# Performance work log

Hardware: AMD Instinct MI355X
Metric: run time of the kernel (lower is better)

## Reference

```python
import jax, jax.numpy as jnp
import numpy as np

HIDDEN = 2048
NUM_HEADS = 32
NUM_GROUPS = 8
HEAD_DIM = HIDDEN // NUM_HEADS          # 64
GROUP_DIM = HEAD_DIM * NUM_GROUPS       # 512
HPG = NUM_HEADS // NUM_GROUPS           # heads per group = 4
B, S = 2, 2048


def setup_inputs() -> dict:
    key = jax.random.key(0)
    ks = jax.random.split(key, 6)
    sd = 1.0 / np.sqrt(HIDDEN)
    return {
        "x": jax.random.normal(ks[0], (B, S, HIDDEN), jnp.float32),
        "mask": jnp.ones((1, 1, S, S), jnp.int32),
        "Wq": jax.random.normal(ks[1], (HIDDEN, HIDDEN), jnp.float32) * sd,
        "bq": jnp.zeros((HIDDEN,), jnp.float32),
        "Wk": jax.random.normal(ks[2], (HIDDEN, GROUP_DIM), jnp.float32) * sd,
        "bk": jnp.zeros((GROUP_DIM,), jnp.float32),
        "Wv": jax.random.normal(ks[3], (HIDDEN, GROUP_DIM), jnp.float32) * sd,
        "bv": jnp.zeros((GROUP_DIM,), jnp.float32),
        "Wo": jax.random.normal(ks[4], (HIDDEN, HIDDEN), jnp.float32) * sd,
        "bo": jnp.zeros((HIDDEN,), jnp.float32),
    }


def reference(x, mask, Wq, bq, Wk, bk, Wv, bv, Wo, bo):
    b, s, _ = x.shape
    # projections
    q = x @ Wq + bq                                        # [B,S,H*d]
    k = x @ Wk + bk                                        # [B,S,G*d]
    v = x @ Wv + bv
    # split heads: q heads are group-major (g, p) to match the torch view
    q = q.reshape(b, s, NUM_GROUPS, HPG, HEAD_DIM)         # [B,S,G,P,d]
    k = k.reshape(b, s, NUM_GROUPS, HEAD_DIM)              # [B,S,G,d]
    v = v.reshape(b, s, NUM_GROUPS, HEAD_DIM)
    scale = 1.0 / np.sqrt(HEAD_DIM).astype(np.float32)
    # grouped attention without materializing repeated K/V
    scores = jnp.einsum('bsgpd,btgd->bgpst', q, k) * scale  # [B,G,P,S,T]
    if mask is not None:
        m = mask[:, :, None]                                # [1,1,1,S,T]
        scores = jnp.where(m == 0, jnp.float32(-1e9), scores)
    weights = jax.nn.softmax(scores, axis=-1)
    out = jnp.einsum('bgpst,btgd->bsgpd', weights, v)       # [B,S,G,P,d]
    out = out.reshape(b, s, HIDDEN)
    return out @ Wo + bo
```

## Files before the change

kernel.cpp:

```cpp
#include <hip/hip_runtime.h>
#include <hip/hip_bf16.h>


#define DEVINL __device__ __forceinline__

typedef __attribute__((ext_vector_type(8))) short bf16x8;
typedef __attribute__((ext_vector_type(4))) float f32x4;

DEVINL unsigned short f2bf(float f) {
  unsigned u = __builtin_bit_cast(unsigned, f);
  u += 0x7fffu + ((u >> 16) & 1u);
  return (unsigned short)(u >> 16);
}

DEVINL unsigned pk2bf(float a, float b) {
  __hip_bfloat162 h = __float22bfloat162_rn(float2{a, b});
  unsigned r;
  __builtin_memcpy(&r, &h, 4);
  return r;
}

DEVINL void gl_lds16(const void* g, void* l) {
  __builtin_amdgcn_global_load_lds(
      (const __attribute__((address_space(1))) void*)g,
      (__attribute__((address_space(3))) void*)l, 16, 0, 0);
}

__global__ __launch_bounds__(256)
void prep_k(const float* __restrict__ x,
            const float* __restrict__ Wq, const float* __restrict__ Wk,
            const float* __restrict__ Wv, const float* __restrict__ Wo,
            const int* __restrict__ mask,
            unsigned short* __restrict__ xb,
            unsigned short* __restrict__ WqT, unsigned short* __restrict__ WkT,
            unsigned short* __restrict__ WvT, unsigned short* __restrict__ WoT,
            int* __restrict__ flags)
{
  __shared__ float tile[64][68];
  __shared__ int fl[4];
  int blk = blockIdx.x;
  const int tid = threadIdx.x;
  if (blk < 4096) {
    size_t base = (size_t)blk * 2048 + tid * 8;
    float4 f0 = *(const float4*)&x[base];
    float4 f1 = *(const float4*)&x[base + 4];
    uint4 o;
    o.x = pk2bf(f0.x, f0.y); o.y = pk2bf(f0.z, f0.w);
    o.z = pk2bf(f1.x, f1.y); o.w = pk2bf(f1.z, f1.w);
    *(uint4*)&xb[base] = o;
    return;
  }
  blk -= 4096;
  if (blk >= 2560) {
    int fb = blk - 2560;
    int qt = fb >> 5, tt = fb & 31;
    bool hz = false;
#pragma unroll
    for (int it = 0; it < 8; ++it) {
      int l = it * 1024 + tid * 4;
      int row = l >> 6, col = l & 63;
      int4 mv = *(const int4*)&mask[(size_t)(qt * 128 + row) * 2048 + tt * 64 + col];
      hz |= (mv.x == 0) | (mv.y == 0) | (mv.z == 0) | (mv.w == 0);
    }
    unsigned long long bal = __ballot(hz);
    if ((tid & 63) == 0) fl[tid >> 6] = (bal != 0ull) ? 1 : 0;
    __syncthreads();
    if (tid == 0) flags[fb] = fl[0] | fl[1] | fl[2] | fl[3];
    return;
  }
  const float* W; unsigned short* WT; int N;
  if (blk < 1024)      { W = Wq; WT = WqT; N = 2048; }
  else if (blk < 1280) { W = Wk; WT = WkT; N = 512;  blk -= 1024; }
  else if (blk < 1536) { W = Wv; WT = WvT; N = 512;  blk -= 1280; }
  else                 { W = Wo; WT = WoT; N = 2048; blk -= 1536; }
  const int kt = blk & 31, nt = blk >> 5;
  const int k0 = kt * 64, n0 = nt * 64;
  const int tr = tid >> 4, tc4 = (tid & 15) * 4;
#pragma unroll
  for (int it = 0; it < 4; ++it) {
    int k = it * 16 + tr;
    float4 v = *(const float4*)&W[(size_t)(k0 + k) * N + n0 + tc4];
    tile[tc4 + 0][k] = v.x; tile[tc4 + 1][k] = v.y;
    tile[tc4 + 2][k] = v.z; tile[tc4 + 3][k] = v.w;
  }
  __syncthreads();
#pragma unroll
  for (int it = 0; it < 4; ++it) {
    int n = it * 16 + tr;
    uint2 o;
    o.x = pk2bf(tile[n][tc4 + 0], tile[n][tc4 + 1]);
    o.y = pk2bf(tile[n][tc4 + 2], tile[n][tc4 + 3]);
    *(uint2*)&WT[(size_t)(n0 + n) * 2048 + k0 + tc4] = o;
  }
}

template<int MODE>
__global__ __launch_bounds__(256)
void mm_k(const unsigned short* __restrict__ A,
          const unsigned short* __restrict__ B1,
          const unsigned short* __restrict__ B2,
          const float* __restrict__ bias1, const float* __restrict__ bias2,
          unsigned short* __restrict__ Ob, unsigned short* __restrict__ Ob2,
          float* __restrict__ Of)
{
  __shared__ __align__(16) unsigned short As[128 * 32];
  __shared__ __align__(16) unsigned short Bs[128 * 32];
  const int tid = threadIdx.x;
  const int lane = tid & 63, w = tid >> 6;
  const int l15 = lane & 15, quad = lane >> 4;
  const int wm = w & 1, wn = w >> 1;
  const int row0 = blockIdx.y * 128;
  const int col0 = blockIdx.x * 128;

  const bool second = (MODE == 1) && (col0 >= 512);
  const unsigned short* Bsrc = second ? B2 : B1;
  const float* bias = second ? bias2 : bias1;
  const int colB = second ? col0 - 512 : col0;

  f32x4 acc[4][4];
#pragma unroll
  for (int mt = 0; mt < 4; ++mt)
#pragma unroll
    for (int nt = 0; nt < 4; ++nt) acc[mt][nt] = (f32x4){0.f, 0.f, 0.f, 0.f};

  const int c0 = tid, c1 = 256 + tid;
  const size_t aoff0 = (size_t)(row0 + (c0 >> 2)) * 2048 + (c0 & 3) * 8;
  const size_t aoff1 = (size_t)(row0 + (c1 >> 2)) * 2048 + (c1 & 3) * 8;
  const size_t boff0 = (size_t)(colB + (c0 >> 2)) * 2048 + (c0 & 3) * 8;
  const size_t boff1 = (size_t)(colB + (c1 >> 2)) * 2048 + (c1 & 3) * 8;

  for (int k0 = 0; k0 < 2048; k0 += 32) {
    gl_lds16(A + aoff0 + k0, As + (size_t)c0 * 8);
    gl_lds16(A + aoff1 + k0, As + (size_t)c1 * 8);
    gl_lds16(Bsrc + boff0 + k0, Bs + (size_t)c0 * 8);
    gl_lds16(Bsrc + boff1 + k0, Bs + (size_t)c1 * 8);
    __syncthreads();
    bf16x8 af[4], bfr[4];
#pragma unroll
    for (int mt = 0; mt < 4; ++mt)
      af[mt] = *(const bf16x8*)&As[(wm * 64 + mt * 16 + l15) * 32 + quad * 8];
#pragma unroll
    for (int nt = 0; nt < 4; ++nt)
      bfr[nt] = *(const bf16x8*)&Bs[(wn * 64 + nt * 16 + l15) * 32 + quad * 8];
#pragma unroll
    for (int mt = 0; mt < 4; ++mt)
#pragma unroll
      for (int nt = 0; nt < 4; ++nt)
        acc[mt][nt] = __builtin_amdgcn_mfma_f32_16x16x32_bf16(
            af[mt], bfr[nt], acc[mt][nt], 0, 0, 0);
    __syncthreads();
  }

  const int rbase = row0 + wm * 64 + quad * 4;
#pragma unroll
  for (int nt = 0; nt < 4; ++nt) {
    const int cg = col0 + wn * 64 + nt * 16 + l15;
    const int cl = colB + wn * 64 + nt * 16 + l15;
    const float bv = bias[MODE == 1 ? cl : cg];
#pragma unroll
    for (int mt = 0; mt < 4; ++mt) {
#pragma unroll
      for (int reg = 0; reg < 4; ++reg) {
        const int r = rbase + mt * 16 + reg;
        const int bb = r >> 11, ss = r & 2047;
        float v = acc[mt][nt][reg] + bv;
        if constexpr (MODE == 0) {
          int g = cg >> 8, p = (cg >> 6) & 3, d = cg & 63;
          Ob[(((size_t)((bb * 8 + g) * 4 + p)) * 2048 + ss) * 64 + d] =
              f2bf(v * 0.1803368801111244f);
        } else if constexpr (MODE == 1) {
          int g = cl >> 6, d = cl & 63;
          if (!second)
            Ob[((size_t)(bb * 8 + g) * 2048 + ss) * 64 + d] = f2bf(v);
          else
            Ob2[((size_t)(bb * 8 + g) * 64 + d) * 2048 + ss] = f2bf(v);
        } else {
          Of[(size_t)r * 2048 + cg] = v;
        }
      }
    }
  }
}

__global__ __launch_bounds__(256)
void attn_k(const unsigned short* __restrict__ qb,
            const unsigned short* __restrict__ kb,
            const unsigned short* __restrict__ vb,
            const int* __restrict__ mask, const int* __restrict__ flags,
            unsigned short* __restrict__ attnb)
{
  __shared__ __align__(16) unsigned short Ks[64 * 64];
  __shared__ __align__(16) unsigned short Vs[64 * 64];
  __shared__ __align__(16) unsigned short Ps[128 * 72];
  const int tid = threadIdx.x;
  const int lane = tid & 63, w = tid >> 6;
  const int l15 = lane & 15, quad = lane >> 4;
  const int q0 = blockIdx.x * 128;
  const int bgp = blockIdx.y;
  const int b = bgp >> 5, bg = bgp >> 2, h = bgp & 31;

  const unsigned short* Qg = qb + (size_t)bgp * 2048 * 64;
  const unsigned short* Kg = kb + (size_t)bg * 2048 * 64;
  const unsigned short* Vg = vb + (size_t)bg * 64 * 2048;

  bf16x8 qf[2][2];
#pragma unroll
  for (int u = 0; u < 2; ++u) {
    const size_t qrow = (size_t)(q0 + w * 32 + u * 16 + l15) * 64;
    qf[u][0] = *(const bf16x8*)&Qg[qrow + quad * 8];
    qf[u][1] = *(const bf16x8*)&Qg[qrow + 32 + quad * 8];
  }

  float m_i[2] = {-3e38f, -3e38f}, l_p[2] = {0.f, 0.f};
  f32x4 acc_o[4][2];
#pragma unroll
  for (int dt = 0; dt < 4; ++dt)
#pragma unroll
    for (int u = 0; u < 2; ++u) acc_o[dt][u] = (f32x4){0.f, 0.f, 0.f, 0.f};

  const int c0 = tid, c1 = 256 + tid;
  const int kr0 = c0 >> 3, kx0 = ((c0 & 7) ^ (kr0 & 7)) * 8;
  const int kr1 = c1 >> 3, kx1 = ((c1 & 7) ^ (kr1 & 7)) * 8;

  for (int t0 = 0; t0 < 2048; t0 += 64) {
    __syncthreads();
    gl_lds16(Kg + (size_t)(t0 + kr0) * 64 + kx0, Ks + (size_t)c0 * 8);
    gl_lds16(Kg + (size_t)(t0 + kr1) * 64 + kx1, Ks + (size_t)c1 * 8);
    gl_lds16(Vg + (size_t)kr0 * 2048 + t0 + kx0, Vs + (size_t)c0 * 8);
    gl_lds16(Vg + (size_t)kr1 * 2048 + t0 + kx1, Vs + (size_t)c1 * 8);
    __syncthreads();

    f32x4 st[2][4];
#pragma unroll
    for (int nt = 0; nt < 4; ++nt) {
      const int trow = nt * 16 + l15, ks = trow & 7;
      bf16x8 k0f = *(const bf16x8*)&Ks[trow * 64 + ((quad ^ ks) * 8)];
      bf16x8 k1f = *(const bf16x8*)&Ks[trow * 64 + (((4 + quad) ^ ks) * 8)];
#pragma unroll
      for (int u = 0; u < 2; ++u) {
        f32x4 z = (f32x4){0.f, 0.f, 0.f, 0.f};
        z = __builtin_amdgcn_mfma_f32_16x16x32_bf16(k0f, qf[u][0], z, 0, 0, 0);
        st[u][nt] = __builtin_amdgcn_mfma_f32_16x16x32_bf16(k1f, qf[u][1], z, 0, 0, 0);
      }
    }

    if (flags[blockIdx.x * 32 + (t0 >> 6)]) {
#pragma unroll
      for (int u = 0; u < 2; ++u) {
        const size_t mrow = (size_t)(q0 + w * 32 + u * 16 + l15) * 2048;
#pragma unroll
        for (int nt = 0; nt < 4; ++nt) {
          int4 mv = *(const int4*)&mask[mrow + t0 + nt * 16 + quad * 4];
          if (mv.x == 0) st[u][nt][0] = -1e30f;
          if (mv.y == 0) st[u][nt][1] = -1e30f;
          if (mv.z == 0) st[u][nt][2] = -1e30f;
          if (mv.w == 0) st[u][nt][3] = -1e30f;
        }
      }
    }

#pragma unroll
    for (int u = 0; u < 2; ++u) {
      float bm = fmaxf(fmaxf(fmaxf(st[u][0][0], st[u][0][1]), fmaxf(st[u][0][2], st[u][0][3])),
                       fmaxf(fmaxf(st[u][1][0], st[u][1][1]), fmaxf(st[u][1][2], st[u][1][3])));
      float bm2 = fmaxf(fmaxf(fmaxf(st[u][2][0], st[u][2][1]), fmaxf(st[u][2][2], st[u][2][3])),
                        fmaxf(fmaxf(st[u][3][0], st[u][3][1]), fmaxf(st[u][3][2], st[u][3][3])));
      bm = fmaxf(bm, bm2);
      bm = fmaxf(bm, __shfl_xor(bm, 16, 64));
      bm = fmaxf(bm, __shfl_xor(bm, 32, 64));
      float mn = fmaxf(m_i[u], bm);
      float alpha = __builtin_amdgcn_exp2f(m_i[u] - mn);
      m_i[u] = mn;
      float sum = 0.f;
#pragma unroll
      for (int nt = 0; nt < 4; ++nt)
#pragma unroll
        for (int reg = 0; reg < 4; ++reg) {
          float p = __builtin_amdgcn_exp2f(st[u][nt][reg] - mn);
          st[u][nt][reg] = p;
          sum += p;
        }
      l_p[u] = l_p[u] * alpha + sum;
#pragma unroll
      for (int dt = 0; dt < 4; ++dt) {
        acc_o[dt][u][0] *= alpha; acc_o[dt][u][1] *= alpha;
        acc_o[dt][u][2] *= alpha; acc_o[dt][u][3] *= alpha;
      }
      const int srow = w * 32 + u * 16 + l15;
#pragma unroll
      for (int nt = 0; nt < 4; ++nt) {
        uint2 pkd;
        pkd.x = pk2bf(st[u][nt][0], st[u][nt][1]);
        pkd.y = pk2bf(st[u][nt][2], st[u][nt][3]);
        *(uint2*)&Ps[srow * 72 + nt * 16 + quad * 4] = pkd;
      }
    }
    asm volatile("s_waitcnt lgkmcnt(0)" ::: "memory");

    bf16x8 pf[2][2];
#pragma unroll
    for (int u = 0; u < 2; ++u) {
      const int srow = w * 32 + u * 16 + l15;
      pf[u][0] = *(const bf16x8*)&Ps[srow * 72 + quad * 8];
      pf[u][1] = *(const bf16x8*)&Ps[srow * 72 + 32 + quad * 8];
    }
#pragma unroll
    for (int dt = 0; dt < 4; ++dt) {
      const int drow = dt * 16 + l15, ks = drow & 7;
      bf16x8 v0 = *(const bf16x8*)&Vs[drow * 64 + ((quad ^ ks) * 8)];
      bf16x8 v1 = *(const bf16x8*)&Vs[drow * 64 + (((4 + quad) ^ ks) * 8)];
#pragma unroll
      for (int u = 0; u < 2; ++u) {
        acc_o[dt][u] = __builtin_amdgcn_mfma_f32_16x16x32_bf16(v0, pf[u][0], acc_o[dt][u], 0, 0, 0);
        acc_o[dt][u] = __builtin_amdgcn_mfma_f32_16x16x32_bf16(v1, pf[u][1], acc_o[dt][u], 0, 0, 0);
      }
    }
  }

#pragma unroll
  for (int u = 0; u < 2; ++u) {
    float l = l_p[u];
    l += __shfl_xor(l, 16, 64);
    l += __shfl_xor(l, 32, 64);
    const float inv = 1.0f / l;
    const int s = q0 + w * 32 + u * 16 + l15;
#pragma unroll
    for (int dt = 0; dt < 4; ++dt) {
      uint2 o;
      o.x = pk2bf(acc_o[dt][u][0] * inv, acc_o[dt][u][1] * inv);
      o.y = pk2bf(acc_o[dt][u][2] * inv, acc_o[dt][u][3] * inv);
      *(uint2*)&attnb[((size_t)(b * 2048 + s)) * 2048 + h * 64 + dt * 16 + quad * 4] = o;
    }
  }
}

extern "C" void kernel_launch(void* const* d_in, const int* in_sizes, int n_in,
                              void* d_out, int out_size, void* d_ws, size_t ws_size,
                              hipStream_t stream)
{
  (void)in_sizes; (void)n_in; (void)out_size; (void)ws_size;
  const float* x  = (const float*)d_in[0];
  const int* mask = (const int*)d_in[1];
  const float* Wq = (const float*)d_in[2];
  const float* bq = (const float*)d_in[3];
  const float* Wk = (const float*)d_in[4];
  const float* bk = (const float*)d_in[5];
  const float* Wv = (const float*)d_in[6];
  const float* bv = (const float*)d_in[7];
  const float* Wo = (const float*)d_in[8];
  const float* bo = (const float*)d_in[9];
  float* out = (float*)d_out;

  unsigned short* xb  = (unsigned short*)d_ws;
  unsigned short* WqT = xb  + 8388608;
  unsigned short* WkT = WqT + 4194304;
  unsigned short* WvT = WkT + 1048576;
  unsigned short* WoT = WvT + 1048576;
  unsigned short* qb  = WoT + 4194304;
  unsigned short* kb  = qb  + 8388608;
  unsigned short* vb  = kb  + 2097152;
  int* flags = (int*)(vb + 2097152);
  unsigned short* attnb = xb;

  dim3 blk(256);
  hipLaunchKernelGGL(prep_k, dim3(7168), blk, 0, stream,
                     x, Wq, Wk, Wv, Wo, mask, xb, WqT, WkT, WvT, WoT, flags);
  hipLaunchKernelGGL((mm_k<0>), dim3(16, 32), blk, 0, stream,
                     xb, WqT, (const unsigned short*)nullptr, bq, (const float*)nullptr,
                     qb, (unsigned short*)nullptr, (float*)nullptr);
  hipLaunchKernelGGL((mm_k<1>), dim3(8, 32), blk, 0, stream,
                     xb, WkT, WvT, bk, bv, kb, vb, (float*)nullptr);
  hipLaunchKernelGGL(attn_k, dim3(16, 64), blk, 0, stream,
                     qb, kb, vb, mask, flags, attnb);
  hipLaunchKernelGGL((mm_k<2>), dim3(16, 32), blk, 0, stream,
                     attnb, WoT, (const unsigned short*)nullptr, bo, (const float*)nullptr,
                     (unsigned short*)nullptr, (unsigned short*)nullptr, out);
}
```

Before: 411.6 us.

## Fuse QKV projection GEMMs, double-buffer attention K/V tiles, skip redundant softmax rescales

The separate Q and KV projection launches are merged into one 24x32-block GEMM over the contiguous WqT/WkT/WvT buffers. Each column block routes its bias and output layout by column range, which removes a launch and fills the GPU better. In attention, K/V tiles are double-buffered in LDS so the next tile's loads are issued while the current one is computed, at the cost of twice the LDS for K and V. The online-softmax rescale of the accumulator and running sum now runs only when some lane's running max increases, using a wave-uniform ballot.

```diff
diff --git a/kernel.cpp b/kernel.cpp
--- a/kernel.cpp
+++ b/kernel.cpp
@@ -94,14 +94,13 @@
   }
 }
 
-template<int MODE>
 __global__ __launch_bounds__(256)
-void mm_k(const unsigned short* __restrict__ A,
-          const unsigned short* __restrict__ B1,
-          const unsigned short* __restrict__ B2,
-          const float* __restrict__ bias1, const float* __restrict__ bias2,
-          unsigned short* __restrict__ Ob, unsigned short* __restrict__ Ob2,
-          float* __restrict__ Of)
+void mm_qkv(const unsigned short* __restrict__ A,
+            const unsigned short* __restrict__ Wt,
+            const float* __restrict__ bq, const float* __restrict__ bk,
+            const float* __restrict__ bv,
+            unsigned short* __restrict__ qb, unsigned short* __restrict__ kb,
+            unsigned short* __restrict__ vb)
 {
   __shared__ __align__(16) unsigned short As[128 * 32];
   __shared__ __align__(16) unsigned short Bs[128 * 32];
@@ -112,11 +111,6 @@
   const int row0 = blockIdx.y * 128;
   const int col0 = blockIdx.x * 128;
 
-  const bool second = (MODE == 1) && (col0 >= 512);
-  const unsigned short* Bsrc = second ? B2 : B1;
-  const float* bias = second ? bias2 : bias1;
-  const int colB = second ? col0 - 512 : col0;
-
   f32x4 acc[4][4];
 #pragma unroll
   for (int mt = 0; mt < 4; ++mt)
@@ -126,14 +120,14 @@
   const int c0 = tid, c1 = 256 + tid;
   const size_t aoff0 = (size_t)(row0 + (c0 >> 2)) * 2048 + (c0 & 3) * 8;
   const size_t aoff1 = (size_t)(row0 + (c1 >> 2)) * 2048 + (c1 & 3) * 8;
-  const size_t boff0 = (size_t)(colB + (c0 >> 2)) * 2048 + (c0 & 3) * 8;
-  const size_t boff1 = (size_t)(colB + (c1 >> 2)) * 2048 + (c1 & 3) * 8;
+  const size_t boff0 = (size_t)(col0 + (c0 >> 2)) * 2048 + (c0 & 3) * 8;
+  const size_t boff1 = (size_t)(col0 + (c1 >> 2)) * 2048 + (c1 & 3) * 8;
 
   for (int k0 = 0; k0 < 2048; k0 += 32) {
     gl_lds16(A + aoff0 + k0, As + (size_t)c0 * 8);
     gl_lds16(A + aoff1 + k0, As + (size_t)c1 * 8);
-    gl_lds16(Bsrc + boff0 + k0, Bs + (size_t)c0 * 8);
-    gl_lds16(Bsrc + boff1 + k0, Bs + (size_t)c1 * 8);
+    gl_lds16(Wt + boff0 + k0, Bs + (size_t)c0 * 8);
+    gl_lds16(Wt + boff1 + k0, Bs + (size_t)c1 * 8);
     __syncthreads();
     bf16x8 af[4], bfr[4];
 #pragma unroll
@@ -155,30 +149,94 @@
 #pragma unroll
   for (int nt = 0; nt < 4; ++nt) {
     const int cg = col0 + wn * 64 + nt * 16 + l15;
-    const int cl = colB + wn * 64 + nt * 16 + l15;
-    const float bv = bias[MODE == 1 ? cl : cg];
 #pragma unroll
     for (int mt = 0; mt < 4; ++mt) {
 #pragma unroll
       for (int reg = 0; reg < 4; ++reg) {
         const int r = rbase + mt * 16 + reg;
         const int bb = r >> 11, ss = r & 2047;
-        float v = acc[mt][nt][reg] + bv;
-        if constexpr (MODE == 0) {
+        float v = acc[mt][nt][reg];
+        if (col0 < 2048) {
+          v += bq[cg];
           int g = cg >> 8, p = (cg >> 6) & 3, d = cg & 63;
-          Ob[(((size_t)((bb * 8 + g) * 4 + p)) * 2048 + ss) * 64 + d] =
+          qb[(((size_t)((bb * 8 + g) * 4 + p)) * 2048 + ss) * 64 + d] =
               f2bf(v * 0.1803368801111244f);
-        } else if constexpr (MODE == 1) {
+        } else if (col0 < 2560) {
+          int cl = cg - 2048;
+          v += bk[cl];
           int g = cl >> 6, d = cl & 63;
-          if (!second)
-            Ob[((size_t)(bb * 8 + g) * 2048 + ss) * 64 + d] = f2bf(v);
-          else
-            Ob2[((size_t)(bb * 8 + g) * 64 + d) * 2048 + ss] = f2bf(v);
+          kb[((size_t)(bb * 8 + g) * 2048 + ss) * 64 + d] = f2bf(v);
         } else {
-          Of[(size_t)r * 2048 + cg] = v;
+          int cl = cg - 2560;
+          v += bv[cl];
+          int g = cl >> 6, d = cl & 63;
+          vb[((size_t)(bb * 8 + g) * 64 + d) * 2048 + ss] = f2bf(v);
         }
       }
     }
+  }
+}
+
+__global__ __launch_bounds__(256)
+void mm_out(const unsigned short* __restrict__ A,
+            const unsigned short* __restrict__ Bt,
+            const float* __restrict__ bias, float* __restrict__ Of)
+{
+  __shared__ __align__(16) unsigned short As[128 * 32];
+  __shared__ __align__(16) unsigned short Bs[128 * 32];
+  const int tid = threadIdx.x;
+  const int lane = tid & 63, w = tid >> 6;
+  const int l15 = lane & 15, quad = lane >> 4;
+  const int wm = w & 1, wn = w >> 1;
+  const int row0 = blockIdx.y * 128;
+  const int col0 = blockIdx.x * 128;
+
+  f32x4 acc[4][4];
+#pragma unroll
+  for (int mt = 0; mt < 4; ++mt)
+#pragma unroll
+    for (int nt = 0; nt < 4; ++nt) acc[mt][nt] = (f32x4){0.f, 0.f, 0.f, 0.f};
+
+  const int c0 = tid, c1 = 256 + tid;
+  const size_t aoff0 = (size_t)(row0 + (c0 >> 2)) * 2048 + (c0 & 3) * 8;
+  const size_t aoff1 = (size_t)(row0 + (c1 >> 2)) * 2048 + (c1 & 3) * 8;
+  const size_t boff0 = (size_t)(col0 + (c0 >> 2)) * 2048 + (c0 & 3) * 8;
+  const size_t boff1 = (size_t)(col0 + (c1 >> 2)) * 2048 + (c1 & 3) * 8;
+
+  for (int k0 = 0; k0 < 2048; k0 += 32) {
+    gl_lds16(A + aoff0 + k0, As + (size_t)c0 * 8);
+    gl_lds16(A + aoff1 + k0, As + (size_t)c1 * 8);
+    gl_lds16(Bt + boff0 + k0, Bs + (size_t)c0 * 8);
+    gl_lds16(Bt + boff1 + k0, Bs + (size_t)c1 * 8);
+    __syncthreads();
+    bf16x8 af[4], bfr[4];
+#pragma unroll
+    for (int mt = 0; mt < 4; ++mt)
+      af[mt] = *(const bf16x8*)&As[(wm * 64 + mt * 16 + l15) * 32 + quad * 8];
+#pragma unroll
+    for (int nt = 0; nt < 4; ++nt)
+      bfr[nt] = *(const bf16x8*)&Bs[(wn * 64 + nt * 16 + l15) * 32 + quad * 8];
+#pragma unroll
+    for (int mt = 0; mt < 4; ++mt)
+#pragma unroll
+      for (int nt = 0; nt < 4; ++nt)
+        acc[mt][nt] = __builtin_amdgcn_mfma_f32_16x16x32_bf16(
+            af[mt], bfr[nt], acc[mt][nt], 0, 0, 0);
+    __syncthreads();
+  }
+
+  const int rbase = row0 + wm * 64 + quad * 4;
+#pragma unroll
+  for (int nt = 0; nt < 4; ++nt) {
+    const int cg = col0 + wn * 64 + nt * 16 + l15;
+    const float bvv = bias[cg];
+#pragma unroll
+    for (int mt = 0; mt < 4; ++mt)
+#pragma unroll
+      for (int reg = 0; reg < 4; ++reg) {
+        const int r = rbase + mt * 16 + reg;
+        Of[(size_t)r * 2048 + cg] = acc[mt][nt][reg] + bvv;
+      }
   }
 }
 
@@ -189,8 +247,8 @@
             const int* __restrict__ mask, const int* __restrict__ flags,
             unsigned short* __restrict__ attnb)
 {
-  __shared__ __align__(16) unsigned short Ks[64 * 64];
-  __shared__ __align__(16) unsigned short Vs[64 * 64];
+  __shared__ __align__(16) unsigned short Ks[2 * 64 * 64];
+  __shared__ __align__(16) unsigned short Vs[2 * 64 * 64];
   __shared__ __align__(16) unsigned short Ps[128 * 72];
   const int tid = threadIdx.x;
   const int lane = tid & 63, w = tid >> 6;
@@ -222,20 +280,32 @@
   const int kr0 = c0 >> 3, kx0 = ((c0 & 7) ^ (kr0 & 7)) * 8;
   const int kr1 = c1 >> 3, kx1 = ((c1 & 7) ^ (kr1 & 7)) * 8;
 
+  gl_lds16(Kg + (size_t)kr0 * 64 + kx0, Ks + (size_t)c0 * 8);
+  gl_lds16(Kg + (size_t)kr1 * 64 + kx1, Ks + (size_t)c1 * 8);
+  gl_lds16(Vg + (size_t)kr0 * 2048 + kx0, Vs + (size_t)c0 * 8);
+  gl_lds16(Vg + (size_t)kr1 * 2048 + kx1, Vs + (size_t)c1 * 8);
+
   for (int t0 = 0; t0 < 2048; t0 += 64) {
-    __syncthreads();
-    gl_lds16(Kg + (size_t)(t0 + kr0) * 64 + kx0, Ks + (size_t)c0 * 8);
-    gl_lds16(Kg + (size_t)(t0 + kr1) * 64 + kx1, Ks + (size_t)c1 * 8);
-    gl_lds16(Vg + (size_t)kr0 * 2048 + t0 + kx0, Vs + (size_t)c0 * 8);
-    gl_lds16(Vg + (size_t)kr1 * 2048 + t0 + kx1, Vs + (size_t)c1 * 8);
-    __syncthreads();
+    const int cur = (t0 >> 6) & 1;
+    const unsigned short* Ksc = Ks + cur * 4096;
+    const unsigned short* Vsc = Vs + cur * 4096;
+    __syncthreads();
+    if (t0 + 64 < 2048) {
+      unsigned short* Ksn = Ks + (cur ^ 1) * 4096;
+      unsigned short* Vsn = Vs + (cur ^ 1) * 4096;
+      const int tn = t0 + 64;
+      gl_lds16(Kg + (size_t)(tn + kr0) * 64 + kx0, Ksn + (size_t)c0 * 8);
+      gl_lds16(Kg + (size_t)(tn + kr1) * 64 + kx1, Ksn + (size_t)c1 * 8);
+      gl_lds16(Vg + (size_t)kr0 * 2048 + tn + kx0, Vsn + (size_t)c0 * 8);
+      gl_lds16(Vg + (size_t)kr1 * 2048 + tn + kx1, Vsn + (size_t)c1 * 8);
+    }
 
     f32x4 st[2][4];
 #pragma unroll
     for (int nt = 0; nt < 4; ++nt) {
       const int trow = nt * 16 + l15, ks = trow & 7;
-      bf16x8 k0f = *(const bf16x8*)&Ks[trow * 64 + ((quad ^ ks) * 8)];
-      bf16x8 k1f = *(const bf16x8*)&Ks[trow * 64 + (((4 + quad) ^ ks) * 8)];
+      bf16x8 k0f = *(const bf16x8*)&Ksc[trow * 64 + ((quad ^ ks) * 8)];
+      bf16x8 k1f = *(const bf16x8*)&Ksc[trow * 64 + (((4 + quad) ^ ks) * 8)];
 #pragma unroll
       for (int u = 0; u < 2; ++u) {
         f32x4 z = (f32x4){0.f, 0.f, 0.f, 0.f};
@@ -268,24 +338,28 @@
       bm = fmaxf(bm, bm2);
       bm = fmaxf(bm, __shfl_xor(bm, 16, 64));
       bm = fmaxf(bm, __shfl_xor(bm, 32, 64));
-      float mn = fmaxf(m_i[u], bm);
-      float alpha = __builtin_amdgcn_exp2f(m_i[u] - mn);
-      m_i[u] = mn;
+      if (__ballot(bm > m_i[u])) {
+        float mn = fmaxf(m_i[u], bm);
+        float alpha = __builtin_amdgcn_exp2f(m_i[u] - mn);
+        m_i[u] = mn;
+        l_p[u] *= alpha;
+#pragma unroll
+        for (int dt = 0; dt < 4; ++dt) {
+          acc_o[dt][u][0] *= alpha; acc_o[dt][u][1] *= alpha;
+          acc_o[dt][u][2] *= alpha; acc_o[dt][u][3] *= alpha;
+        }
+      }
+      const float mm = m_i[u];
       float sum = 0.f;
 #pragma unroll
       for (int nt = 0; nt < 4; ++nt)
 #pragma unroll
         for (int reg = 0; reg < 4; ++reg) {
-          float p = __builtin_amdgcn_exp2f(st[u][nt][reg] - mn);
+          float p = __builtin_amdgcn_exp2f(st[u][nt][reg] - mm);
           st[u][nt][reg] = p;
           sum += p;
         }
-      l_p[u] = l_p[u] * alpha + sum;
-#pragma unroll
-      for (int dt = 0; dt < 4; ++dt) {
-        acc_o[dt][u][0] *= alpha; acc_o[dt][u][1] *= alpha;
-        acc_o[dt][u][2] *= alpha; acc_o[dt][u][3] *= alpha;
-      }
+      l_p[u] += sum;
       const int srow = w * 32 + u * 16 + l15;
 #pragma unroll
       for (int nt = 0; nt < 4; ++nt) {
@@ -307,8 +381,8 @@
 #pragma unroll
     for (int dt = 0; dt < 4; ++dt) {
       const int drow = dt * 16 + l15, ks = drow & 7;
-      bf16x8 v0 = *(const bf16x8*)&Vs[drow * 64 + ((quad ^ ks) * 8)];
-      bf16x8 v1 = *(const bf16x8*)&Vs[drow * 64 + (((4 + quad) ^ ks) * 8)];
+      bf16x8 v0 = *(const bf16x8*)&Vsc[drow * 64 + ((quad ^ ks) * 8)];
+      bf16x8 v1 = *(const bf16x8*)&Vsc[drow * 64 + (((4 + quad) ^ ks) * 8)];
 #pragma unroll
       for (int u = 0; u < 2; ++u) {
         acc_o[dt][u] = __builtin_amdgcn_mfma_f32_16x16x32_bf16(v0, pf[u][0], acc_o[dt][u], 0, 0, 0);
@@ -365,14 +439,10 @@
   dim3 blk(256);
   hipLaunchKernelGGL(prep_k, dim3(7168), blk, 0, stream,
                      x, Wq, Wk, Wv, Wo, mask, xb, WqT, WkT, WvT, WoT, flags);
-  hipLaunchKernelGGL((mm_k<0>), dim3(16, 32), blk, 0, stream,
-                     xb, WqT, (const unsigned short*)nullptr, bq, (const float*)nullptr,
-                     qb, (unsigned short*)nullptr, (float*)nullptr);
-  hipLaunchKernelGGL((mm_k<1>), dim3(8, 32), blk, 0, stream,
-                     xb, WkT, WvT, bk, bv, kb, vb, (float*)nullptr);
+  hipLaunchKernelGGL(mm_qkv, dim3(24, 32), blk, 0, stream,
+                     xb, WqT, bq, bk, bv, qb, kb, vb);
   hipLaunchKernelGGL(attn_k, dim3(16, 64), blk, 0, stream,
                      qb, kb, vb, mask, flags, attnb);
-  hipLaunchKernelGGL((mm_k<2>), dim3(16, 32), blk, 0, stream,
-                     attnb, WoT, (const unsigned short*)nullptr, bo, (const float*)nullptr,
-                     (unsigned short*)nullptr, (unsigned short*)nullptr, out);
-}
+  hipLaunchKernelGGL(mm_out, dim3(16, 32), blk, 0, stream,
+                     attnb, WoT, bo, out);
+}
```

New measurement: 393.6 us. 1.05x faster.
